# Kernel tuning notes

Hardware: AMD Instinct MI355X
Metric: run time of the kernel (lower is better)

Reference implementation:

```python
import jax, jax.numpy as jnp
import numpy as np

B, S, D = 4, 4096, 2048
K, H = 64, 32
HD = K // H  # 2
LN_EPS = 1e-5


def setup_inputs() -> dict:
    key = jax.random.key(0)
    ks = jax.random.split(key, 8)
    def xavier(k, shape):
        fan_in, fan_out = shape[1], shape[0]
        lim = float(np.sqrt(6.0 / (fan_in + fan_out)))
        return jax.random.uniform(k, shape, jnp.float32, -lim, lim)
    return {
        "x": jax.random.normal(ks[0], (B, S, D), jnp.float32),
        "norm_w": jnp.ones((D,), jnp.float32),
        "norm_b": jnp.zeros((D,), jnp.float32),
        "qkv_w": xavier(ks[1], (3 * K, D)),
        "qkv_b": jnp.zeros((3 * K,), jnp.float32),
        "fm_w": xavier(ks[2], (HD, HD)),
        "fm_b": jnp.zeros((HD,), jnp.float32),
        "out_w": xavier(ks[3], (D, K)),
        "out_b": jnp.zeros((D,), jnp.float32),
    }


def reference(x, norm_w, norm_b, qkv_w, qkv_b, fm_w, fm_b, out_w, out_b):
    # LayerNorm
    mu = jnp.mean(x, axis=-1, keepdims=True)
    var = jnp.var(x, axis=-1, keepdims=True)
    xn = (x - mu) * jax.lax.rsqrt(var + LN_EPS) * norm_w + norm_b
    # QKV projection: [B,S,3K]
    qkv = xn @ qkv_w.T + qkv_b
    q, k, v = jnp.split(qkv, 3, axis=-1)
    # [B,S,K] -> [B,H,S,hd]
    def heads(t):
        return t.reshape(B, S, H, HD).transpose(0, 2, 1, 3)
    q, k, v = heads(q), heads(k), heads(v)
    # feature map: ReLU(Linear)
    q = jax.nn.relu(q @ fm_w.T + fm_b)
    k = jax.nn.relu(k @ fm_w.T + fm_b)
    # linear attention: kv state [B,H,hd,hd]
    kv = jnp.einsum('bhsd,bhse->bhde', k, v)
    attn = jnp.einsum('bhsd,bhde->bhse', q, kv)
    k_sum = jnp.sum(k, axis=2)                      # [B,H,hd]
    q_k_sum = jnp.einsum('bhsd,bhd->bhs', q, k_sum)[..., None]
    attn = attn / (q_k_sum + 1e-8)
    # merge heads -> [B,S,K]
    attn = attn.transpose(0, 2, 1, 3).reshape(B, S, K)
    out = attn @ out_w.T + out_b
    return x + out
```

## Files before the change

### kernel.cpp

```cpp
#include <hip/hip_runtime.h>
#include <hip/hip_bf16.h>
#include <stdint.h>

typedef unsigned short ushort_t;

#define BB 4
#define SS 4096
#define DD 2048
#define KKC 64
#define HH 32
#define NT (BB*SS)
#define NQKV 192
#define QB 64

typedef float f32x4 __attribute__((ext_vector_type(4)));
typedef short s16x8 __attribute__((ext_vector_type(8)));

__device__ __forceinline__ ushort_t f2bf(float f) {
    union { float f; uint32_t u; } c; c.f = f;
    uint32_t u = c.u + 0x7fffu + ((c.u >> 16) & 1u);
    return (ushort_t)(u >> 16);
}
__device__ __forceinline__ float bf2f(ushort_t b) {
    union { uint32_t u; float f; } c; c.u = (uint32_t)b << 16; return c.f;
}

__device__ __forceinline__ uint32_t cvtpk(float lo, float hi) {
    uint32_t r;
    asm("v_cvt_pk_bf16_f32 %0, %1, %2" : "=v"(r) : "v"(lo), "v"(hi));
    return r;
}

__device__ __forceinline__ void mfma16(f32x4& d, s16x8 a, s16x8 b) {
    asm volatile("v_mfma_f32_16x16x32_bf16 %0, %1, %2, %0" : "+v"(d) : "v"(a), "v"(b));
}

__device__ __forceinline__ void gload_lds16(const void* gsrc, void* ldst) {
    __builtin_amdgcn_global_load_lds(
        (const __attribute__((address_space(1))) unsigned int*)gsrc,
        (__attribute__((address_space(3))) unsigned int*)ldst,
        16, 0, 0);
}

__global__ __launch_bounds__(256) void k_pre(
    const float* __restrict__ qkv_w, const float* __restrict__ nw,
    const float* __restrict__ out_w,
    ushort_t* __restrict__ W1, ushort_t* __restrict__ W2) {
    int E = blockIdx.x * 256 + threadIdx.x;
    if (E < 49152) {
        int lane = E & 63; int rest = E >> 6;
        int f = rest % 12, g = rest / 12;
        int col = f * 16 + (lane & 15);
        int k0 = g * 32 + 8 * (lane >> 4);
        const float* src = qkv_w + (size_t)col * DD + k0;
        const float* wp = nw + k0;
        union { ushort_t u[8]; uint4 v; } cv;
        #pragma unroll
        for (int e = 0; e < 8; ++e) cv.u[e] = f2bf(src[e] * wp[e]);
        *(uint4*)(W1 + (size_t)E * 8) = cv.v;
    } else {
        int E2 = E - 49152;
        int lane = E2 & 63; int rest = E2 >> 6;
        int kk = rest & 1, F = rest >> 1;
        int n = F * 16 + (lane & 15);
        int k0 = kk * 32 + 8 * (lane >> 4);
        const float* src = out_w + (size_t)n * KKC + k0;
        union { ushort_t u[8]; uint4 v; } cv;
        #pragma unroll
        for (int e = 0; e < 8; ++e) cv.u[e] = f2bf(src[e]);
        *(uint4*)(W2 + (size_t)E2 * 8) = cv.v;
    }
}

__global__ __launch_bounds__(256) void k_colsum(
    const float* __restrict__ qkv_w, const float* __restrict__ nw,
    const float* __restrict__ nb, const float* __restrict__ qkv_b,
    float* __restrict__ S, float* __restrict__ qb2) {
    int col = blockIdx.x * 4 + (threadIdx.x >> 6);
    int lane = threadIdx.x & 63;
    float s = 0.f, qb = 0.f;
    for (int j = 0; j < 32; ++j) {
        int k = j * 64 + lane;
        float w = qkv_w[(size_t)col * DD + k];
        s += bf2f(f2bf(w * nw[k]));
        qb += nb[k] * w;
    }
    #pragma unroll
    for (int off = 32; off >= 1; off >>= 1) {
        s += __shfl_xor(s, off);
        qb += __shfl_xor(qb, off);
    }
    if (lane == 0) { S[col] = s; qb2[col] = qb + qkv_b[col]; }
}

__global__ __launch_bounds__(512, 2) void k_qkv(
    const float* __restrict__ x, const ushort_t* __restrict__ W1,
    const float* __restrict__ S, const float* __restrict__ qb2,
    const float* __restrict__ fm_w, const float* __restrict__ fm_b,
    float* __restrict__ qfeat,
    float* __restrict__ kvpart)
{
    __shared__ __align__(16) union {
        float xs[2][QB * 16 * 4];
        float cep[QB][NQKV];
    } sm;
    __shared__ float kvred[32][16][6];
    __shared__ float stats2[2][QB][2];
    __shared__ float stats[QB][2];

    const int tid = threadIdx.x;
    const int wave = tid >> 6, lane = tid & 63;
    const int rg = wave & 3, ch = wave >> 2;
    const int m0 = blockIdx.x * QB;

    const int rloc = rg * 16 + (lane & 15);
    const int q4 = lane >> 4;
    const int swz = rloc & 7;

    const int idx0 = wave * 64 + lane;
    const int idx1 = 512 + idx0;
    const int row0 = idx0 >> 4, row1 = idx1 >> 4;
    const size_t xg0 = (size_t)(m0 + row0) * DD + (((idx0 & 15) ^ (row0 & 7)) * 4);
    const size_t xg1 = (size_t)(m0 + row1) * DD + (((idx1 & 15) ^ (row1 & 7)) * 4);
    const int xd0 = (wave * 64) * 16;
    const int xd1 = (512 + wave * 64) * 16;

    const s16x8* __restrict__ Wp = (const s16x8*)W1;
    const int fbase = ch * 6;

    f32x4 acc[6];
    #pragma unroll
    for (int j = 0; j < 6; ++j) acc[j] = (f32x4){0.f, 0.f, 0.f, 0.f};
    float st1 = 0.f, st2 = 0.f;

#define STAGE_X(T, BUF) do { \
        gload_lds16(x + xg0 + (size_t)(T) * 64, (char*)sm.xs[BUF] + xd0); \
        gload_lds16(x + xg1 + (size_t)(T) * 64, (char*)sm.xs[BUF] + xd1); \
    } while (0)

#define LOAD_B(T, DST) do { \
        _Pragma("unroll") \
        for (int kb = 0; kb < 2; ++kb) { \
            _Pragma("unroll") \
            for (int j = 0; j < 6; ++j) \
                DST[kb][j] = Wp[(((size_t)((T) * 2 + kb) * 12) + fbase + j) * 64 + lane]; \
        } \
    } while (0)

#define AFRAG(BUF, DOSTATS) \
        s16x8 afr0, afr1; \
        { \
            const float* base = sm.xs[BUF] + rloc * 64; \
            int sg0 = 2 * q4, sg1 = 8 + 2 * q4; \
            float4 a0 = *(const float4*)(base + ((sg0    ) ^ swz) * 4); \
            float4 a1 = *(const float4*)(base + ((sg0 + 1) ^ swz) * 4); \
            float4 b0 = *(const float4*)(base + ((sg1    ) ^ swz) * 4); \
            float4 b1 = *(const float4*)(base + ((sg1 + 1) ^ swz) * 4); \
            if (DOSTATS) { \
                st1 += a0.x+a0.y+a0.z+a0.w + a1.x+a1.y+a1.z+a1.w \
                     + b0.x+b0.y+b0.z+b0.w + b1.x+b1.y+b1.z+b1.w; \
                st2 += a0.x*a0.x+a0.y*a0.y+a0.z*a0.z+a0.w*a0.w \
                     + a1.x*a1.x+a1.y*a1.y+a1.z*a1.z+a1.w*a1.w \
                     + b0.x*b0.x+b0.y*b0.y+b0.z*b0.z+b0.w*b0.w \
                     + b1.x*b1.x+b1.y*b1.y+b1.z*b1.z+b1.w*b1.w; \
            } \
            union { uint32_t w[4]; s16x8 v; } c0, c1; \
            c0.w[0] = cvtpk(a0.x, a0.y); c0.w[1] = cvtpk(a0.z, a0.w); \
            c0.w[2] = cvtpk(a1.x, a1.y); c0.w[3] = cvtpk(a1.z, a1.w); \
            c1.w[0] = cvtpk(b0.x, b0.y); c1.w[1] = cvtpk(b0.z, b0.w); \
            c1.w[2] = cvtpk(b1.x, b1.y); c1.w[3] = cvtpk(b1.z, b1.w); \
            afr0 = c0.v; afr1 = c1.v; \
        }

    s16x8 bA[2][6], bB[2][6];

    STAGE_X(0, 0);
    LOAD_B(0, bA);

    for (int tp = 0; tp < 16; ++tp) {
        const int t0 = 2 * tp, t1 = 2 * tp + 1;
        __syncthreads();
        STAGE_X(t0 + 1, 1);
        LOAD_B(t0 + 1, bB);
        {
            AFRAG(0, (ch == 0));
            #pragma unroll
            for (int j = 0; j < 6; ++j) {
                mfma16(acc[j], afr0, bA[0][j]);
                mfma16(acc[j], afr1, bA[1][j]);
            }
        }
        __syncthreads();
        if (t1 < 31) {
            STAGE_X(t1 + 1, 0);
            LOAD_B(t1 + 1, bA);
        }
        {
            AFRAG(1, (ch == 1));
            #pragma unroll
            for (int j = 0; j < 6; ++j) {
                mfma16(acc[j], afr0, bB[0][j]);
                mfma16(acc[j], afr1, bB[1][j]);
            }
        }
    }

    st1 += __shfl_xor(st1, 16); st2 += __shfl_xor(st2, 16);
    st1 += __shfl_xor(st1, 32); st2 += __shfl_xor(st2, 32);
    if (lane < 16) { stats2[ch][rloc][0] = st1; stats2[ch][rloc][1] = st2; }
    __syncthreads();

    #pragma unroll
    for (int j = 0; j < 6; ++j) {
        int col = (fbase + j) * 16 + (lane & 15);
        int rbase = rg * 16 + (lane >> 4) * 4;
        #pragma unroll
        for (int r = 0; r < 4; ++r)
            sm.cep[rbase + r][col] = acc[j][r];
    }
    if (tid < QB) {
        float s1 = stats2[0][tid][0] + stats2[1][tid][0];
        float s2 = stats2[0][tid][1] + stats2[1][tid][1];
        float mu = s1 * (1.f / DD);
        float var = s2 * (1.f / DD) - mu * mu;
        stats[tid][0] = mu;
        stats[tid][1] = rsqrtf(var + 1e-5f);
    }
    __syncthreads();

    const int h = tid & 31, gg = tid >> 5;
    const float fm00 = fm_w[0], fm01 = fm_w[1], fm10 = fm_w[2], fm11 = fm_w[3];
    const float fb0 = fm_b[0], fb1 = fm_b[1];
    const float Sq0 = S[2*h],      Sq1 = S[2*h+1],      cq0 = qb2[2*h],      cq1 = qb2[2*h+1];
    const float Sk0 = S[64+2*h],   Sk1 = S[64+2*h+1],   ck0 = qb2[64+2*h],   ck1 = qb2[64+2*h+1];
    const float Sv0 = S[128+2*h],  Sv1 = S[128+2*h+1],  cv0 = qb2[128+2*h],  cv1 = qb2[128+2*h+1];
    float kv00=0, kv01=0, kv10=0, kv11=0, ks0=0, ks1=0;
    #pragma unroll
    for (int i = 0; i < 4; ++i) {
        int tt = gg * 4 + i;
        float mu = stats[tt][0], rs = stats[tt][1];
        float f = mu * rs;
        float q0 = rs * sm.cep[tt][2*h]      - f * Sq0 + cq0;
        float q1 = rs * sm.cep[tt][2*h+1]    - f * Sq1 + cq1;
        float k0 = rs * sm.cep[tt][64+2*h]   - f * Sk0 + ck0;
        float k1 = rs * sm.cep[tt][64+2*h+1] - f * Sk1 + ck1;
        float v0 = rs * sm.cep[tt][128+2*h]  - f * Sv0 + cv0;
        float v1 = rs * sm.cep[tt][128+2*h+1]- f * Sv1 + cv1;
        float qp0 = fmaxf(fm00*q0 + fm01*q1 + fb0, 0.f);
        float qp1 = fmaxf(fm10*q0 + fm11*q1 + fb1, 0.f);
        float kp0 = fmaxf(fm00*k0 + fm01*k1 + fb0, 0.f);
        float kp1 = fmaxf(fm10*k0 + fm11*k1 + fb1, 0.f);
        *(float2*)(qfeat + (size_t)(m0 + tt) * KKC + 2*h) = make_float2(qp0, qp1);
        kv00 += kp0*v0; kv01 += kp0*v1; kv10 += kp1*v0; kv11 += kp1*v1;
        ks0 += kp0; ks1 += kp1;
    }
    kvred[h][gg][0]=kv00; kvred[h][gg][1]=kv01; kvred[h][gg][2]=kv10;
    kvred[h][gg][3]=kv11; kvred[h][gg][4]=ks0;  kvred[h][gg][5]=ks1;
    __syncthreads();
    if (tid < 192) {
        int h2 = tid / 6, j = tid % 6;
        float s = 0.f;
        #pragma unroll
        for (int g2 = 0; g2 < 16; ++g2) s += kvred[h2][g2][j];
        kvpart[(size_t)blockIdx.x * 192 + tid] = s;
    }
#undef STAGE_X
#undef LOAD_B
#undef AFRAG
}

__global__ void k_red(const float* __restrict__ kvpart, float* __restrict__ kvstate) {
    int idx = blockIdx.x * 256 + threadIdx.x;
    if (idx >= BB * HH * 6) return;
    int b = idx / 192, r = idx % 192;
    float s = 0.f;
    for (int blk = 0; blk < 64; ++blk)
        s += kvpart[(size_t)(b * 64 + blk) * 192 + r];
    kvstate[idx] = s;
}

#define CEP_STRIDE 260
__global__ __launch_bounds__(512, 4) void k_out(
    const float* __restrict__ qfeat, const float* __restrict__ kvstate,
    const ushort_t* __restrict__ W2, const float* __restrict__ out_b,
    const float* __restrict__ x, float* __restrict__ out) {
    __shared__ float skv[192];
    __shared__ __align__(16) float cep[32 * CEP_STRIDE];
    const int tid = threadIdx.x, wave = tid >> 6, lane = tid & 63;
    const int rg = wave & 1, cq = wave >> 1;
    const int mb = blockIdx.x >> 1, nb = blockIdx.x & 1;
    const int m0 = mb * 32;
    const int n0 = nb * 1024;
    const int b = m0 >> 12;
    if (tid < 192) skv[tid] = kvstate[b * 192 + tid];

    const int arow = m0 + rg * 16 + (lane & 15);
    const int ksub = 8 * (lane >> 4);
    float4 qa0 = *(const float4*)(qfeat + (size_t)arow * KKC + ksub);
    float4 qa1 = *(const float4*)(qfeat + (size_t)arow * KKC + ksub + 4);
    float4 qb0 = *(const float4*)(qfeat + (size_t)arow * KKC + 32 + ksub);
    float4 qb1 = *(const float4*)(qfeat + (size_t)arow * KKC + 32 + ksub + 4);
    __syncthreads();

    union { ushort_t u[8]; s16x8 v; } ca, cb;
    {
        float qs[8] = {qa0.x,qa0.y,qa0.z,qa0.w,qa1.x,qa1.y,qa1.z,qa1.w};
        float rs[8] = {qb0.x,qb0.y,qb0.z,qb0.w,qb1.x,qb1.y,qb1.z,qb1.w};
        #pragma unroll
        for (int e = 0; e < 8; e += 2) {
            int h = (ksub + e) >> 1;
            const float* kv = skv + h * 6;
            float q0 = qs[e], q1 = qs[e+1];
            float inv = 1.f / (q0 * kv[4] + q1 * kv[5] + 1e-8f);
            ca.u[e]   = f2bf((q0 * kv[0] + q1 * kv[2]) * inv);
            ca.u[e+1] = f2bf((q0 * kv[1] + q1 * kv[3]) * inv);
            const float* kw = skv + (h + 16) * 6;
            float p0 = rs[e], p1 = rs[e+1];
            float iw = 1.f / (p0 * kw[4] + p1 * kw[5] + 1e-8f);
            cb.u[e]   = f2bf((p0 * kw[0] + p1 * kw[2]) * iw);
            cb.u[e+1] = f2bf((p0 * kw[1] + p1 * kw[3]) * iw);
        }
    }

    f32x4 acc[16];
    #pragma unroll
    for (int j = 0; j < 16; ++j) acc[j] = (f32x4){0.f, 0.f, 0.f, 0.f};
    #pragma unroll
    for (int j = 0; j < 16; ++j) {
        int Fg = (n0 >> 4) + cq + 4 * j;
        s16x8 b0 = *(const s16x8*)(W2 + ((size_t)(Fg * 2 + 0) * 64 + lane) * 8);
        s16x8 b1 = *(const s16x8*)(W2 + ((size_t)(Fg * 2 + 1) * 64 + lane) * 8);
        mfma16(acc[j], ca.v, b0);
        mfma16(acc[j], cb.v, b1);
    }

    const int wrow = rg * 16 + 4 * (lane >> 4);
    #pragma unroll
    for (int n = 0; n < 4; ++n) {
        #pragma unroll
        for (int i = 0; i < 4; ++i) {
            int col = cq * 16 + i * 64 + (lane & 15);
            #pragma unroll
            for (int r = 0; r < 4; ++r)
                cep[(wrow + r) * CEP_STRIDE + col] = acc[4 * n + i][r];
        }
        __syncthreads();
        #pragma unroll
        for (int p = 0; p < 4; ++p) {
            int row = p * 8 + (tid >> 6);
            int c4 = tid & 63;
            float4 c = *(const float4*)(cep + row * CEP_STRIDE + c4 * 4);
            int gcol = n0 + n * 256 + c4 * 4;
            size_t off = (size_t)(m0 + row) * DD + gcol;
            float4 xr = *(const float4*)(x + off);
            float4 ob = *(const float4*)(out_b + gcol);
            float4 o;
            o.x = c.x + ob.x + xr.x; o.y = c.y + ob.y + xr.y;
            o.z = c.z + ob.z + xr.z; o.w = c.w + ob.w + xr.w;
            *(float4*)(out + off) = o;
        }
        __syncthreads();
    }
}

extern "C" void kernel_launch(void* const* d_in, const int* in_sizes, int n_in,
                              void* d_out, int out_size, void* d_ws, size_t ws_size,
                              hipStream_t stream) {
    const float* x     = (const float*)d_in[0];
    const float* nw    = (const float*)d_in[1];
    const float* nb    = (const float*)d_in[2];
    const float* qkv_w = (const float*)d_in[3];
    const float* qkv_b = (const float*)d_in[4];
    const float* fm_w  = (const float*)d_in[5];
    const float* fm_b  = (const float*)d_in[6];
    const float* out_w = (const float*)d_in[7];
    const float* out_b = (const float*)d_in[8];
    float* out = (float*)d_out;

    char* ws = (char*)d_ws;
    ushort_t* W1 = (ushort_t*)ws;     ws += (size_t)NQKV * DD * 2;
    ushort_t* W2 = (ushort_t*)ws;     ws += (size_t)DD * KKC * 2;
    float* qfeat = (float*)ws;        ws += (size_t)NT * KKC * 4;
    float* kvpart = (float*)ws;       ws += (size_t)256 * 192 * 4;
    float* kvstate = (float*)ws;      ws += (size_t)BB * HH * 6 * 4;
    float* Svec = (float*)ws;         ws += (size_t)NQKV * 4;
    float* qb2 = (float*)ws;          ws += (size_t)NQKV * 4;

    k_pre<<<256, 256, 0, stream>>>(qkv_w, nw, out_w, W1, W2);
    k_colsum<<<48, 256, 0, stream>>>(qkv_w, nw, nb, qkv_b, Svec, qb2);
    k_qkv<<<NT / QB, 512, 0, stream>>>(x, W1, Svec, qb2, fm_w, fm_b, qfeat, kvpart);
    k_red<<<3, 256, 0, stream>>>(kvpart, kvstate);
    k_out<<<(NT / 32) * 2, 512, 0, stream>>>(qfeat, kvstate, W2, out_b, x, out);
}
```

Measured before the change: 127.8 us.

## Shrink QKV row tile to 16 rows with 4-wave blocks for more parallelism

The fused LayerNorm+QKV kernel now handles 16 rows per block with 256 threads instead of 64 rows with 512 threads. That gives 1024 blocks instead of 256. Each wave now owns 3 of the 12 output column tiles. LayerNorm statistics are split round-robin across the four waves by k-step. The partial kv buffers and the reduction kernel are resized to match. The aim is better spread across CUs and better latency hiding on the x stream, at the cost of each block re-reading the full bf16 QKV weight, which multiplies weight traffic through the cache by four.

```diff
diff --git a/kernel.cpp b/kernel.cpp
--- a/kernel.cpp
+++ b/kernel.cpp
@@ -11,7 +11,7 @@
 #define HH 32
 #define NT (BB*SS)
 #define NQKV 192
-#define QB 64
+#define QB 16
 
 typedef float f32x4 __attribute__((ext_vector_type(4)));
 typedef short s16x8 __attribute__((ext_vector_type(8)));
@@ -93,7 +93,7 @@
     if (lane == 0) { S[col] = s; qb2[col] = qb + qkv_b[col]; }
 }
 
-__global__ __launch_bounds__(512, 2) void k_qkv(
+__global__ __launch_bounds__(256, 4) void k_qkv(
     const float* __restrict__ x, const ushort_t* __restrict__ W1,
     const float* __restrict__ S, const float* __restrict__ qb2,
     const float* __restrict__ fm_w, const float* __restrict__ fm_b,
@@ -101,48 +101,43 @@
     float* __restrict__ kvpart)
 {
     __shared__ __align__(16) union {
-        float xs[2][QB * 16 * 4];
+        float xs[2][QB * 64];
         float cep[QB][NQKV];
     } sm;
-    __shared__ float kvred[32][16][6];
-    __shared__ float stats2[2][QB][2];
+    __shared__ float kvred[32][8][6];
+    __shared__ float stats4[4][QB][2];
     __shared__ float stats[QB][2];
 
     const int tid = threadIdx.x;
     const int wave = tid >> 6, lane = tid & 63;
-    const int rg = wave & 3, ch = wave >> 2;
+    const int ch = wave;
     const int m0 = blockIdx.x * QB;
 
-    const int rloc = rg * 16 + (lane & 15);
+    const int rloc = lane & 15;
     const int q4 = lane >> 4;
     const int swz = rloc & 7;
 
-    const int idx0 = wave * 64 + lane;
-    const int idx1 = 512 + idx0;
-    const int row0 = idx0 >> 4, row1 = idx1 >> 4;
-    const size_t xg0 = (size_t)(m0 + row0) * DD + (((idx0 & 15) ^ (row0 & 7)) * 4);
-    const size_t xg1 = (size_t)(m0 + row1) * DD + (((idx1 & 15) ^ (row1 & 7)) * 4);
+    const int row0 = tid >> 4;
+    const int slot0 = (tid & 15) ^ (row0 & 7);
+    const size_t xg0 = (size_t)(m0 + row0) * DD + slot0 * 4;
     const int xd0 = (wave * 64) * 16;
-    const int xd1 = (512 + wave * 64) * 16;
 
     const s16x8* __restrict__ Wp = (const s16x8*)W1;
-    const int fbase = ch * 6;
-
-    f32x4 acc[6];
-    #pragma unroll
-    for (int j = 0; j < 6; ++j) acc[j] = (f32x4){0.f, 0.f, 0.f, 0.f};
+    const int fbase = ch * 3;
+
+    f32x4 acc[3];
+    #pragma unroll
+    for (int j = 0; j < 3; ++j) acc[j] = (f32x4){0.f, 0.f, 0.f, 0.f};
     float st1 = 0.f, st2 = 0.f;
 
-#define STAGE_X(T, BUF) do { \
-        gload_lds16(x + xg0 + (size_t)(T) * 64, (char*)sm.xs[BUF] + xd0); \
-        gload_lds16(x + xg1 + (size_t)(T) * 64, (char*)sm.xs[BUF] + xd1); \
-    } while (0)
+#define STAGE_X(T, BUF) \
+    gload_lds16(x + xg0 + (size_t)(T) * 64, (char*)sm.xs[BUF] + xd0)
 
 #define LOAD_B(T, DST) do { \
         _Pragma("unroll") \
         for (int kb = 0; kb < 2; ++kb) { \
             _Pragma("unroll") \
-            for (int j = 0; j < 6; ++j) \
+            for (int j = 0; j < 3; ++j) \
                 DST[kb][j] = Wp[(((size_t)((T) * 2 + kb) * 12) + fbase + j) * 64 + lane]; \
         } \
     } while (0)
@@ -172,7 +167,7 @@
             afr0 = c0.v; afr1 = c1.v; \
         }
 
-    s16x8 bA[2][6], bB[2][6];
+    s16x8 bA[2][3], bB[2][3];
 
     STAGE_X(0, 0);
     LOAD_B(0, bA);
@@ -183,9 +178,9 @@
         STAGE_X(t0 + 1, 1);
         LOAD_B(t0 + 1, bB);
         {
-            AFRAG(0, (ch == 0));
+            AFRAG(0, ((t0 & 3) == ch));
             #pragma unroll
-            for (int j = 0; j < 6; ++j) {
+            for (int j = 0; j < 3; ++j) {
                 mfma16(acc[j], afr0, bA[0][j]);
                 mfma16(acc[j], afr1, bA[1][j]);
             }
@@ -196,9 +191,9 @@
             LOAD_B(t1 + 1, bA);
         }
         {
-            AFRAG(1, (ch == 1));
+            AFRAG(1, ((t1 & 3) == ch));
             #pragma unroll
-            for (int j = 0; j < 6; ++j) {
+            for (int j = 0; j < 3; ++j) {
                 mfma16(acc[j], afr0, bB[0][j]);
                 mfma16(acc[j], afr1, bB[1][j]);
             }
@@ -207,20 +202,20 @@
 
     st1 += __shfl_xor(st1, 16); st2 += __shfl_xor(st2, 16);
     st1 += __shfl_xor(st1, 32); st2 += __shfl_xor(st2, 32);
-    if (lane < 16) { stats2[ch][rloc][0] = st1; stats2[ch][rloc][1] = st2; }
+    if (lane < 16) { stats4[ch][lane][0] = st1; stats4[ch][lane][1] = st2; }
     __syncthreads();
 
     #pragma unroll
-    for (int j = 0; j < 6; ++j) {
+    for (int j = 0; j < 3; ++j) {
         int col = (fbase + j) * 16 + (lane & 15);
-        int rbase = rg * 16 + (lane >> 4) * 4;
+        int rbase = (lane >> 4) * 4;
         #pragma unroll
         for (int r = 0; r < 4; ++r)
             sm.cep[rbase + r][col] = acc[j][r];
     }
     if (tid < QB) {
-        float s1 = stats2[0][tid][0] + stats2[1][tid][0];
-        float s2 = stats2[0][tid][1] + stats2[1][tid][1];
+        float s1 = stats4[0][tid][0] + stats4[1][tid][0] + stats4[2][tid][0] + stats4[3][tid][0];
+        float s2 = stats4[0][tid][1] + stats4[1][tid][1] + stats4[2][tid][1] + stats4[3][tid][1];
         float mu = s1 * (1.f / DD);
         float var = s2 * (1.f / DD) - mu * mu;
         stats[tid][0] = mu;
@@ -236,8 +231,8 @@
     const float Sv0 = S[128+2*h],  Sv1 = S[128+2*h+1],  cv0 = qb2[128+2*h],  cv1 = qb2[128+2*h+1];
     float kv00=0, kv01=0, kv10=0, kv11=0, ks0=0, ks1=0;
     #pragma unroll
-    for (int i = 0; i < 4; ++i) {
-        int tt = gg * 4 + i;
+    for (int i = 0; i < 2; ++i) {
+        int tt = gg * 2 + i;
         float mu = stats[tt][0], rs = stats[tt][1];
         float f = mu * rs;
         float q0 = rs * sm.cep[tt][2*h]      - f * Sq0 + cq0;
@@ -261,7 +256,7 @@
         int h2 = tid / 6, j = tid % 6;
         float s = 0.f;
         #pragma unroll
-        for (int g2 = 0; g2 < 16; ++g2) s += kvred[h2][g2][j];
+        for (int g2 = 0; g2 < 8; ++g2) s += kvred[h2][g2][j];
         kvpart[(size_t)blockIdx.x * 192 + tid] = s;
     }
 #undef STAGE_X
@@ -274,8 +269,8 @@
     if (idx >= BB * HH * 6) return;
     int b = idx / 192, r = idx % 192;
     float s = 0.f;
-    for (int blk = 0; blk < 64; ++blk)
-        s += kvpart[(size_t)(b * 64 + blk) * 192 + r];
+    for (int blk = 0; blk < 256; ++blk)
+        s += kvpart[(size_t)(b * 256 + blk) * 192 + r];
     kvstate[idx] = s;
 }
 
@@ -381,14 +376,14 @@
     ushort_t* W1 = (ushort_t*)ws;     ws += (size_t)NQKV * DD * 2;
     ushort_t* W2 = (ushort_t*)ws;     ws += (size_t)DD * KKC * 2;
     float* qfeat = (float*)ws;        ws += (size_t)NT * KKC * 4;
-    float* kvpart = (float*)ws;       ws += (size_t)256 * 192 * 4;
+    float* kvpart = (float*)ws;       ws += (size_t)1024 * 192 * 4;
     float* kvstate = (float*)ws;      ws += (size_t)BB * HH * 6 * 4;
     float* Svec = (float*)ws;         ws += (size_t)NQKV * 4;
     float* qb2 = (float*)ws;          ws += (size_t)NQKV * 4;
 
     k_pre<<<256, 256, 0, stream>>>(qkv_w, nw, out_w, W1, W2);
     k_colsum<<<48, 256, 0, stream>>>(qkv_w, nw, nb, qkv_b, Svec, qb2);
-    k_qkv<<<NT / QB, 512, 0, stream>>>(x, W1, Svec, qb2, fm_w, fm_b, qfeat, kvpart);
+    k_qkv<<<NT / QB, 256, 0, stream>>>(x, W1, Svec, qb2, fm_w, fm_b, qfeat, kvpart);
     k_red<<<3, 256, 0, stream>>>(kvpart, kvstate);
     k_out<<<(NT / 32) * 2, 512, 0, stream>>>(qfeat, kvstate, W2, out_b, x, out);
 }
```

Result: slower. 139.9 us (+9.5%).

## Stage QKV weights through LDS with triple-buffered async pipeline

Applied to the files above, without the earlier changes.

The QKV GEMM kernel now stages both the bf16 weight tile and the x tile into LDS through direct global-to-LDS loads, using three dynamic-shared-memory buffers and a vmcnt-based wait instead of two buffers plus register-held weight fragments. This is meant to keep two tiles in flight ahead of compute and cut VGPR pressure from the prefetched weight registers. In exchange it uses about 120 KB of LDS per block, so only one block fits per CU, and the launch bounds no longer request two blocks per SM. The epilogue reuses the dynamic LDS region for the accumulator scratch.

```diff
diff --git a/kernel.cpp b/kernel.cpp
--- a/kernel.cpp
+++ b/kernel.cpp
@@ -12,6 +12,9 @@
 #define NT (BB*SS)
 #define NQKV 192
 #define QB 64
+
+#define BUFSZ 40960
+#define XOFF  24576
 
 typedef float f32x4 __attribute__((ext_vector_type(4)));
 typedef short s16x8 __attribute__((ext_vector_type(8)));
@@ -93,17 +96,14 @@
     if (lane == 0) { S[col] = s; qb2[col] = qb + qkv_b[col]; }
 }
 
-__global__ __launch_bounds__(512, 2) void k_qkv(
+__global__ __launch_bounds__(512) void k_qkv(
     const float* __restrict__ x, const ushort_t* __restrict__ W1,
     const float* __restrict__ S, const float* __restrict__ qb2,
     const float* __restrict__ fm_w, const float* __restrict__ fm_b,
     float* __restrict__ qfeat,
     float* __restrict__ kvpart)
 {
-    __shared__ __align__(16) union {
-        float xs[2][QB * 16 * 4];
-        float cep[QB][NQKV];
-    } sm;
+    extern __shared__ __align__(16) char dynlds[];
     __shared__ float kvred[32][16][6];
     __shared__ float stats2[2][QB][2];
     __shared__ float stats[QB][2];
@@ -116,107 +116,97 @@
     const int rloc = rg * 16 + (lane & 15);
     const int q4 = lane >> 4;
     const int swz = rloc & 7;
+    const int fbase = ch * 6;
 
     const int idx0 = wave * 64 + lane;
     const int idx1 = 512 + idx0;
     const int row0 = idx0 >> 4, row1 = idx1 >> 4;
     const size_t xg0 = (size_t)(m0 + row0) * DD + (((idx0 & 15) ^ (row0 & 7)) * 4);
     const size_t xg1 = (size_t)(m0 + row1) * DD + (((idx1 & 15) ^ (row1 & 7)) * 4);
-    const int xd0 = (wave * 64) * 16;
-    const int xd1 = (512 + wave * 64) * 16;
-
-    const s16x8* __restrict__ Wp = (const s16x8*)W1;
-    const int fbase = ch * 6;
+    const int xd0 = idx0 * 16 - lane * 16;
+    const int xd1 = idx1 * 16 - lane * 16;
 
     f32x4 acc[6];
     #pragma unroll
     for (int j = 0; j < 6; ++j) acc[j] = (f32x4){0.f, 0.f, 0.f, 0.f};
     float st1 = 0.f, st2 = 0.f;
 
-#define STAGE_X(T, BUF) do { \
-        gload_lds16(x + xg0 + (size_t)(T) * 64, (char*)sm.xs[BUF] + xd0); \
-        gload_lds16(x + xg1 + (size_t)(T) * 64, (char*)sm.xs[BUF] + xd1); \
+#define STAGE(T, OB) do { \
+        char* bB_ = dynlds + (OB); \
+        char* bX_ = dynlds + (OB) + XOFF; \
+        _Pragma("unroll") \
+        for (int i_ = 0; i_ < 3; ++i_) { \
+            int eb_ = i_ * 512 + wave * 64; \
+            gload_lds16((const char*)W1 + ((size_t)(T) * 1536 + eb_ + lane) * 16, \
+                        bB_ + eb_ * 16); \
+        } \
+        gload_lds16(x + xg0 + (size_t)(T) * 64, bX_ + xd0); \
+        gload_lds16(x + xg1 + (size_t)(T) * 64, bX_ + xd1); \
     } while (0)
 
-#define LOAD_B(T, DST) do { \
+#define STEP_BODY(OC, T) do { \
+        const s16x8* bb_ = (const s16x8*)(dynlds + (OC)); \
+        const float* xb_ = (const float*)(dynlds + (OC) + XOFF) + rloc * 64; \
+        const bool doStats_ = (((T) & 1) == ch); \
+        s16x8 afr0_, afr1_; \
+        { \
+            int sg0_ = 2 * q4, sg1_ = 8 + 2 * q4; \
+            float4 a0_ = *(const float4*)(xb_ + ((sg0_    ) ^ swz) * 4); \
+            float4 a1_ = *(const float4*)(xb_ + ((sg0_ + 1) ^ swz) * 4); \
+            float4 b0_ = *(const float4*)(xb_ + ((sg1_    ) ^ swz) * 4); \
+            float4 b1_ = *(const float4*)(xb_ + ((sg1_ + 1) ^ swz) * 4); \
+            if (doStats_) { \
+                st1 += a0_.x+a0_.y+a0_.z+a0_.w + a1_.x+a1_.y+a1_.z+a1_.w \
+                     + b0_.x+b0_.y+b0_.z+b0_.w + b1_.x+b1_.y+b1_.z+b1_.w; \
+                st2 += a0_.x*a0_.x+a0_.y*a0_.y+a0_.z*a0_.z+a0_.w*a0_.w \
+                     + a1_.x*a1_.x+a1_.y*a1_.y+a1_.z*a1_.z+a1_.w*a1_.w \
+                     + b0_.x*b0_.x+b0_.y*b0_.y+b0_.z*b0_.z+b0_.w*b0_.w \
+                     + b1_.x*b1_.x+b1_.y*b1_.y+b1_.z*b1_.z+b1_.w*b1_.w; \
+            } \
+            union { uint32_t w[4]; s16x8 v; } c0_, c1_; \
+            c0_.w[0] = cvtpk(a0_.x, a0_.y); c0_.w[1] = cvtpk(a0_.z, a0_.w); \
+            c0_.w[2] = cvtpk(a1_.x, a1_.y); c0_.w[3] = cvtpk(a1_.z, a1_.w); \
+            c1_.w[0] = cvtpk(b0_.x, b0_.y); c1_.w[1] = cvtpk(b0_.z, b0_.w); \
+            c1_.w[2] = cvtpk(b1_.x, b1_.y); c1_.w[3] = cvtpk(b1_.z, b1_.w); \
+            afr0_ = c0_.v; afr1_ = c1_.v; \
+        } \
         _Pragma("unroll") \
-        for (int kb = 0; kb < 2; ++kb) { \
-            _Pragma("unroll") \
-            for (int j = 0; j < 6; ++j) \
-                DST[kb][j] = Wp[(((size_t)((T) * 2 + kb) * 12) + fbase + j) * 64 + lane]; \
+        for (int j_ = 0; j_ < 6; ++j_) { \
+            s16x8 w0_ = bb_[(fbase + j_) * 64 + lane]; \
+            s16x8 w1_ = bb_[(12 + fbase + j_) * 64 + lane]; \
+            mfma16(acc[j_], afr0_, w0_); \
+            mfma16(acc[j_], afr1_, w1_); \
         } \
     } while (0)
 
-#define AFRAG(BUF, DOSTATS) \
-        s16x8 afr0, afr1; \
-        { \
-            const float* base = sm.xs[BUF] + rloc * 64; \
-            int sg0 = 2 * q4, sg1 = 8 + 2 * q4; \
-            float4 a0 = *(const float4*)(base + ((sg0    ) ^ swz) * 4); \
-            float4 a1 = *(const float4*)(base + ((sg0 + 1) ^ swz) * 4); \
-            float4 b0 = *(const float4*)(base + ((sg1    ) ^ swz) * 4); \
-            float4 b1 = *(const float4*)(base + ((sg1 + 1) ^ swz) * 4); \
-            if (DOSTATS) { \
-                st1 += a0.x+a0.y+a0.z+a0.w + a1.x+a1.y+a1.z+a1.w \
-                     + b0.x+b0.y+b0.z+b0.w + b1.x+b1.y+b1.z+b1.w; \
-                st2 += a0.x*a0.x+a0.y*a0.y+a0.z*a0.z+a0.w*a0.w \
-                     + a1.x*a1.x+a1.y*a1.y+a1.z*a1.z+a1.w*a1.w \
-                     + b0.x*b0.x+b0.y*b0.y+b0.z*b0.z+b0.w*b0.w \
-                     + b1.x*b1.x+b1.y*b1.y+b1.z*b1.z+b1.w*b1.w; \
-            } \
-            union { uint32_t w[4]; s16x8 v; } c0, c1; \
-            c0.w[0] = cvtpk(a0.x, a0.y); c0.w[1] = cvtpk(a0.z, a0.w); \
-            c0.w[2] = cvtpk(a1.x, a1.y); c0.w[3] = cvtpk(a1.z, a1.w); \
-            c1.w[0] = cvtpk(b0.x, b0.y); c1.w[1] = cvtpk(b0.z, b0.w); \
-            c1.w[2] = cvtpk(b1.x, b1.y); c1.w[3] = cvtpk(b1.z, b1.w); \
-            afr0 = c0.v; afr1 = c1.v; \
-        }
-
-    s16x8 bA[2][6], bB[2][6];
-
-    STAGE_X(0, 0);
-    LOAD_B(0, bA);
-
-    for (int tp = 0; tp < 16; ++tp) {
-        const int t0 = 2 * tp, t1 = 2 * tp + 1;
-        __syncthreads();
-        STAGE_X(t0 + 1, 1);
-        LOAD_B(t0 + 1, bB);
-        {
-            AFRAG(0, (ch == 0));
-            #pragma unroll
-            for (int j = 0; j < 6; ++j) {
-                mfma16(acc[j], afr0, bA[0][j]);
-                mfma16(acc[j], afr1, bA[1][j]);
-            }
-        }
-        __syncthreads();
-        if (t1 < 31) {
-            STAGE_X(t1 + 1, 0);
-            LOAD_B(t1 + 1, bA);
-        }
-        {
-            AFRAG(1, (ch == 1));
-            #pragma unroll
-            for (int j = 0; j < 6; ++j) {
-                mfma16(acc[j], afr0, bB[0][j]);
-                mfma16(acc[j], afr1, bB[1][j]);
-            }
-        }
-    }
+    STAGE(0, 0);
+    STAGE(1, BUFSZ);
+
+    unsigned oc = 0, on = BUFSZ, on2 = 2 * BUFSZ;
+    for (int t = 0; t < 31; ++t) {
+        asm volatile("s_waitcnt vmcnt(5)" ::: "memory");
+        __builtin_amdgcn_s_barrier();
+        if (t < 30) STAGE(t + 2, on2);
+        STEP_BODY(oc, t);
+        unsigned tmp = oc; oc = on; on = on2; on2 = tmp;
+    }
+    asm volatile("s_waitcnt vmcnt(0)" ::: "memory");
+    __builtin_amdgcn_s_barrier();
+    STEP_BODY(oc, 31);
 
     st1 += __shfl_xor(st1, 16); st2 += __shfl_xor(st2, 16);
     st1 += __shfl_xor(st1, 32); st2 += __shfl_xor(st2, 32);
     if (lane < 16) { stats2[ch][rloc][0] = st1; stats2[ch][rloc][1] = st2; }
     __syncthreads();
 
+    float (*cep)[NQKV] = (float (*)[NQKV])dynlds;
     #pragma unroll
     for (int j = 0; j < 6; ++j) {
         int col = (fbase + j) * 16 + (lane & 15);
         int rbase = rg * 16 + (lane >> 4) * 4;
         #pragma unroll
         for (int r = 0; r < 4; ++r)
-            sm.cep[rbase + r][col] = acc[j][r];
+            cep[rbase + r][col] = acc[j][r];
     }
     if (tid < QB) {
         float s1 = stats2[0][tid][0] + stats2[1][tid][0];
@@ -240,12 +230,12 @@
         int tt = gg * 4 + i;
         float mu = stats[tt][0], rs = stats[tt][1];
         float f = mu * rs;
-        float q0 = rs * sm.cep[tt][2*h]      - f * Sq0 + cq0;
-        float q1 = rs * sm.cep[tt][2*h+1]    - f * Sq1 + cq1;
-        float k0 = rs * sm.cep[tt][64+2*h]   - f * Sk0 + ck0;
-        float k1 = rs * sm.cep[tt][64+2*h+1] - f * Sk1 + ck1;
-        float v0 = rs * sm.cep[tt][128+2*h]  - f * Sv0 + cv0;
-        float v1 = rs * sm.cep[tt][128+2*h+1]- f * Sv1 + cv1;
+        float q0 = rs * cep[tt][2*h]      - f * Sq0 + cq0;
+        float q1 = rs * cep[tt][2*h+1]    - f * Sq1 + cq1;
+        float k0 = rs * cep[tt][64+2*h]   - f * Sk0 + ck0;
+        float k1 = rs * cep[tt][64+2*h+1] - f * Sk1 + ck1;
+        float v0 = rs * cep[tt][128+2*h]  - f * Sv0 + cv0;
+        float v1 = rs * cep[tt][128+2*h+1]- f * Sv1 + cv1;
         float qp0 = fmaxf(fm00*q0 + fm01*q1 + fb0, 0.f);
         float qp1 = fmaxf(fm10*q0 + fm11*q1 + fb1, 0.f);
         float kp0 = fmaxf(fm00*k0 + fm01*k1 + fb0, 0.f);
@@ -264,9 +254,8 @@
         for (int g2 = 0; g2 < 16; ++g2) s += kvred[h2][g2][j];
         kvpart[(size_t)blockIdx.x * 192 + tid] = s;
     }
-#undef STAGE_X
-#undef LOAD_B
-#undef AFRAG
+#undef STAGE
+#undef STEP_BODY
 }
 
 __global__ void k_red(const float* __restrict__ kvpart, float* __restrict__ kvstate) {
@@ -386,9 +375,12 @@
     float* Svec = (float*)ws;         ws += (size_t)NQKV * 4;
     float* qb2 = (float*)ws;          ws += (size_t)NQKV * 4;
 
+    hipFuncSetAttribute((const void*)k_qkv,
+                        hipFuncAttributeMaxDynamicSharedMemorySize, 3 * BUFSZ);
+
     k_pre<<<256, 256, 0, stream>>>(qkv_w, nw, out_w, W1, W2);
     k_colsum<<<48, 256, 0, stream>>>(qkv_w, nw, nb, qkv_b, Svec, qb2);
-    k_qkv<<<NT / QB, 512, 0, stream>>>(x, W1, Svec, qb2, fm_w, fm_b, qfeat, kvpart);
+    k_qkv<<<NT / QB, 512, 3 * BUFSZ, stream>>>(x, W1, Svec, qb2, fm_w, fm_b, qfeat, kvpart);
     k_red<<<3, 256, 0, stream>>>(kvpart, kvstate);
     k_out<<<(NT / 32) * 2, 512, 0, stream>>>(qfeat, kvstate, W2, out_b, x, out);
 }
```

Result: faster. 124.1 us (-2.9%).

## Replace LDS-staged x loads with per-wave register prefetch and merge small kernels

Applied to the files above, without the earlier changes.

The QKV kernel no longer stages fp32 x through shared memory with async global-to-LDS loads and block-wide barriers. Each wave now loads its own 16 rows into registers, computes the LayerNorm stats there, converts to bf16 and writes a private swizzled double buffer, so the main loop has no __syncthreads. The column-sum kernel is folded into the weight-prep kernel, and the kv reduction kernel is removed: each k_out block sums the 64 partials itself. This cuts two launches and the per-tile barriers, at the cost of more registers and redundant kv reduction work in every k_out block.

```diff
diff --git a/kernel.cpp b/kernel.cpp
--- a/kernel.cpp
+++ b/kernel.cpp
@@ -35,62 +35,55 @@
     asm volatile("v_mfma_f32_16x16x32_bf16 %0, %1, %2, %0" : "+v"(d) : "v"(a), "v"(b));
 }
 
-__device__ __forceinline__ void gload_lds16(const void* gsrc, void* ldst) {
-    __builtin_amdgcn_global_load_lds(
-        (const __attribute__((address_space(1))) unsigned int*)gsrc,
-        (__attribute__((address_space(3))) unsigned int*)ldst,
-        16, 0, 0);
-}
-
 __global__ __launch_bounds__(256) void k_pre(
     const float* __restrict__ qkv_w, const float* __restrict__ nw,
+    const float* __restrict__ nb, const float* __restrict__ qkv_b,
     const float* __restrict__ out_w,
-    ushort_t* __restrict__ W1, ushort_t* __restrict__ W2) {
-    int E = blockIdx.x * 256 + threadIdx.x;
-    if (E < 49152) {
-        int lane = E & 63; int rest = E >> 6;
-        int f = rest % 12, g = rest / 12;
-        int col = f * 16 + (lane & 15);
-        int k0 = g * 32 + 8 * (lane >> 4);
-        const float* src = qkv_w + (size_t)col * DD + k0;
-        const float* wp = nw + k0;
-        union { ushort_t u[8]; uint4 v; } cv;
-        #pragma unroll
-        for (int e = 0; e < 8; ++e) cv.u[e] = f2bf(src[e] * wp[e]);
-        *(uint4*)(W1 + (size_t)E * 8) = cv.v;
+    ushort_t* __restrict__ W1, ushort_t* __restrict__ W2,
+    float* __restrict__ S, float* __restrict__ qb2) {
+    int bid = blockIdx.x;
+    if (bid < 256) {
+        int E = bid * 256 + threadIdx.x;
+        if (E < 49152) {
+            int lane = E & 63; int rest = E >> 6;
+            int f = rest % 12, g = rest / 12;
+            int col = f * 16 + (lane & 15);
+            int k0 = g * 32 + 8 * (lane >> 4);
+            const float* src = qkv_w + (size_t)col * DD + k0;
+            const float* wp = nw + k0;
+            union { ushort_t u[8]; uint4 v; } cv;
+            #pragma unroll
+            for (int e = 0; e < 8; ++e) cv.u[e] = f2bf(src[e] * wp[e]);
+            *(uint4*)(W1 + (size_t)E * 8) = cv.v;
+        } else {
+            int E2 = E - 49152;
+            int lane = E2 & 63; int rest = E2 >> 6;
+            int kk = rest & 1, F = rest >> 1;
+            int n = F * 16 + (lane & 15);
+            int k0 = kk * 32 + 8 * (lane >> 4);
+            const float* src = out_w + (size_t)n * KKC + k0;
+            union { ushort_t u[8]; uint4 v; } cv;
+            #pragma unroll
+            for (int e = 0; e < 8; ++e) cv.u[e] = f2bf(src[e]);
+            *(uint4*)(W2 + (size_t)E2 * 8) = cv.v;
+        }
     } else {
-        int E2 = E - 49152;
-        int lane = E2 & 63; int rest = E2 >> 6;
-        int kk = rest & 1, F = rest >> 1;
-        int n = F * 16 + (lane & 15);
-        int k0 = kk * 32 + 8 * (lane >> 4);
-        const float* src = out_w + (size_t)n * KKC + k0;
-        union { ushort_t u[8]; uint4 v; } cv;
-        #pragma unroll
-        for (int e = 0; e < 8; ++e) cv.u[e] = f2bf(src[e]);
-        *(uint4*)(W2 + (size_t)E2 * 8) = cv.v;
-    }
-}
-
-__global__ __launch_bounds__(256) void k_colsum(
-    const float* __restrict__ qkv_w, const float* __restrict__ nw,
-    const float* __restrict__ nb, const float* __restrict__ qkv_b,
-    float* __restrict__ S, float* __restrict__ qb2) {
-    int col = blockIdx.x * 4 + (threadIdx.x >> 6);
-    int lane = threadIdx.x & 63;
-    float s = 0.f, qb = 0.f;
-    for (int j = 0; j < 32; ++j) {
-        int k = j * 64 + lane;
-        float w = qkv_w[(size_t)col * DD + k];
-        s += bf2f(f2bf(w * nw[k]));
-        qb += nb[k] * w;
-    }
-    #pragma unroll
-    for (int off = 32; off >= 1; off >>= 1) {
-        s += __shfl_xor(s, off);
-        qb += __shfl_xor(qb, off);
-    }
-    if (lane == 0) { S[col] = s; qb2[col] = qb + qkv_b[col]; }
+        int col = (bid - 256) * 4 + (threadIdx.x >> 6);
+        int lane = threadIdx.x & 63;
+        float s = 0.f, qb = 0.f;
+        for (int j = 0; j < 32; ++j) {
+            int k = j * 64 + lane;
+            float w = qkv_w[(size_t)col * DD + k];
+            s += bf2f(f2bf(w * nw[k]));
+            qb += nb[k] * w;
+        }
+        #pragma unroll
+        for (int off = 32; off >= 1; off >>= 1) {
+            s += __shfl_xor(s, off);
+            qb += __shfl_xor(qb, off);
+        }
+        if (lane == 0) { S[col] = s; qb2[col] = qb + qkv_b[col]; }
+    }
 }
 
 __global__ __launch_bounds__(512, 2) void k_qkv(
@@ -101,130 +94,127 @@
     float* __restrict__ kvpart)
 {
     __shared__ __align__(16) union {
-        float xs[2][QB * 16 * 4];
+        ushort_t xb[8][2][16][64];
         float cep[QB][NQKV];
     } sm;
     __shared__ float kvred[32][16][6];
-    __shared__ float stats2[2][QB][2];
     __shared__ float stats[QB][2];
 
     const int tid = threadIdx.x;
     const int wave = tid >> 6, lane = tid & 63;
     const int rg = wave & 3, ch = wave >> 2;
     const int m0 = blockIdx.x * QB;
-
-    const int rloc = rg * 16 + (lane & 15);
-    const int q4 = lane >> 4;
-    const int swz = rloc & 7;
-
-    const int idx0 = wave * 64 + lane;
-    const int idx1 = 512 + idx0;
-    const int row0 = idx0 >> 4, row1 = idx1 >> 4;
-    const size_t xg0 = (size_t)(m0 + row0) * DD + (((idx0 & 15) ^ (row0 & 7)) * 4);
-    const size_t xg1 = (size_t)(m0 + row1) * DD + (((idx1 & 15) ^ (row1 & 7)) * 4);
-    const int xd0 = (wave * 64) * 16;
-    const int xd1 = (512 + wave * 64) * 16;
-
+    const int fbase = ch * 6;
+    const int l15 = lane & 15, q4 = lane >> 4;
+    const bool doStats = (ch == 0);
+
+    const float* xbase = x + (size_t)(m0 + rg * 16 + q4) * DD + l15 * 4;
+    int wb[4];
+    #pragma unroll
+    for (int i = 0; i < 4; ++i) {
+        int r = i * 4 + q4;
+        wb[i] = r * 128 + ((l15 >> 1) ^ (r & 7)) * 16 + (l15 & 1) * 8;
+    }
     const s16x8* __restrict__ Wp = (const s16x8*)W1;
-    const int fbase = ch * 6;
 
     f32x4 acc[6];
     #pragma unroll
     for (int j = 0; j < 6; ++j) acc[j] = (f32x4){0.f, 0.f, 0.f, 0.f};
-    float st1 = 0.f, st2 = 0.f;
-
-#define STAGE_X(T, BUF) do { \
-        gload_lds16(x + xg0 + (size_t)(T) * 64, (char*)sm.xs[BUF] + xd0); \
-        gload_lds16(x + xg1 + (size_t)(T) * 64, (char*)sm.xs[BUF] + xd1); \
-    } while (0)
-
-#define LOAD_B(T, DST) do { \
-        _Pragma("unroll") \
-        for (int kb = 0; kb < 2; ++kb) { \
-            _Pragma("unroll") \
-            for (int j = 0; j < 6; ++j) \
-                DST[kb][j] = Wp[(((size_t)((T) * 2 + kb) * 12) + fbase + j) * 64 + lane]; \
+    float st1[4] = {0.f, 0.f, 0.f, 0.f}, st2[4] = {0.f, 0.f, 0.f, 0.f};
+
+#define LOADX(T, X) do { \
+        _Pragma("unroll") \
+        for (int i_ = 0; i_ < 4; ++i_) \
+            X[i_] = *(const float4*)(xbase + (size_t)(i_ * 4) * DD + (T) * 64); \
+    } while (0)
+
+#define LOADB(T, D) do { \
+        _Pragma("unroll") \
+        for (int kb_ = 0; kb_ < 2; ++kb_) \
+        { _Pragma("unroll") \
+          for (int cf_ = 0; cf_ < 6; ++cf_) \
+            D[kb_][cf_] = Wp[((size_t)(2 * (T) + kb_) * 12 + fbase + cf_) * 64 + lane]; } \
+    } while (0)
+
+#define CVTW(T, X) do { \
+        char* xbw_ = (char*)&sm.xb[wave][(T) & 1][0][0]; \
+        _Pragma("unroll") \
+        for (int i_ = 0; i_ < 4; ++i_) { \
+            if (doStats) { \
+                st1[i_] += X[i_].x + X[i_].y + X[i_].z + X[i_].w; \
+                st2[i_] += X[i_].x*X[i_].x + X[i_].y*X[i_].y \
+                         + X[i_].z*X[i_].z + X[i_].w*X[i_].w; \
+            } \
+            uint2 w_; \
+            w_.x = cvtpk(X[i_].x, X[i_].y); \
+            w_.y = cvtpk(X[i_].z, X[i_].w); \
+            *(uint2*)(xbw_ + wb[i_]) = w_; \
         } \
     } while (0)
 
-#define AFRAG(BUF, DOSTATS) \
-        s16x8 afr0, afr1; \
-        { \
-            const float* base = sm.xs[BUF] + rloc * 64; \
-            int sg0 = 2 * q4, sg1 = 8 + 2 * q4; \
-            float4 a0 = *(const float4*)(base + ((sg0    ) ^ swz) * 4); \
-            float4 a1 = *(const float4*)(base + ((sg0 + 1) ^ swz) * 4); \
-            float4 b0 = *(const float4*)(base + ((sg1    ) ^ swz) * 4); \
-            float4 b1 = *(const float4*)(base + ((sg1 + 1) ^ swz) * 4); \
-            if (DOSTATS) { \
-                st1 += a0.x+a0.y+a0.z+a0.w + a1.x+a1.y+a1.z+a1.w \
-                     + b0.x+b0.y+b0.z+b0.w + b1.x+b1.y+b1.z+b1.w; \
-                st2 += a0.x*a0.x+a0.y*a0.y+a0.z*a0.z+a0.w*a0.w \
-                     + a1.x*a1.x+a1.y*a1.y+a1.z*a1.z+a1.w*a1.w \
-                     + b0.x*b0.x+b0.y*b0.y+b0.z*b0.z+b0.w*b0.w \
-                     + b1.x*b1.x+b1.y*b1.y+b1.z*b1.z+b1.w*b1.w; \
-            } \
-            union { uint32_t w[4]; s16x8 v; } c0, c1; \
-            c0.w[0] = cvtpk(a0.x, a0.y); c0.w[1] = cvtpk(a0.z, a0.w); \
-            c0.w[2] = cvtpk(a1.x, a1.y); c0.w[3] = cvtpk(a1.z, a1.w); \
-            c1.w[0] = cvtpk(b0.x, b0.y); c1.w[1] = cvtpk(b0.z, b0.w); \
-            c1.w[2] = cvtpk(b1.x, b1.y); c1.w[3] = cvtpk(b1.z, b1.w); \
-            afr0 = c0.v; afr1 = c1.v; \
-        }
-
-    s16x8 bA[2][6], bB[2][6];
-
-    STAGE_X(0, 0);
-    LOAD_B(0, bA);
+#define AREAD(T, AF) do { \
+        const char* xbr_ = (const char*)&sm.xb[wave][(T) & 1][0][0]; \
+        _Pragma("unroll") \
+        for (int kb_ = 0; kb_ < 2; ++kb_) \
+            AF[kb_] = *(const s16x8*)(xbr_ + l15 * 128 + (((kb_ * 4 + q4) ^ (l15 & 7)) << 4)); \
+    } while (0)
+
+#define MM(AF, D) do { \
+        _Pragma("unroll") \
+        for (int kb_ = 0; kb_ < 2; ++kb_) \
+        { _Pragma("unroll") \
+          for (int cf_ = 0; cf_ < 6; ++cf_) \
+            mfma16(acc[cf_], AF[kb_], D[kb_][cf_]); } \
+    } while (0)
+
+    float4 xA[4], xB[4];
+    s16x8 Ba[2][6], Bb[2][6], af[2];
+
+    LOADX(0, xA);
+    LOADB(0, Ba);
+    CVTW(0, xA);
 
     for (int tp = 0; tp < 16; ++tp) {
-        const int t0 = 2 * tp, t1 = 2 * tp + 1;
-        __syncthreads();
-        STAGE_X(t0 + 1, 1);
-        LOAD_B(t0 + 1, bB);
-        {
-            AFRAG(0, (ch == 0));
-            #pragma unroll
-            for (int j = 0; j < 6; ++j) {
-                mfma16(acc[j], afr0, bA[0][j]);
-                mfma16(acc[j], afr1, bA[1][j]);
+        const int t0 = 2 * tp, t1 = t0 + 1;
+        LOADX(t1, xB); LOADB(t1, Bb);
+        AREAD(t0, af); MM(af, Ba);
+        CVTW(t1, xB);
+        if (t1 < 31) { LOADX(t1 + 1, xA); LOADB(t1 + 1, Ba); }
+        AREAD(t1, af); MM(af, Bb);
+        if (t1 < 31) CVTW(t1 + 1, xA);
+    }
+#undef LOADX
+#undef LOADB
+#undef CVTW
+#undef AREAD
+#undef MM
+
+    if (doStats) {
+        #pragma unroll
+        for (int i = 0; i < 4; ++i) {
+            float s1 = st1[i], s2 = st2[i];
+            s1 += __shfl_xor(s1, 1); s2 += __shfl_xor(s2, 1);
+            s1 += __shfl_xor(s1, 2); s2 += __shfl_xor(s2, 2);
+            s1 += __shfl_xor(s1, 4); s2 += __shfl_xor(s2, 4);
+            s1 += __shfl_xor(s1, 8); s2 += __shfl_xor(s2, 8);
+            if (l15 == 0) {
+                int row = rg * 16 + i * 4 + q4;
+                float mu = s1 * (1.f / DD);
+                float var = s2 * (1.f / DD) - mu * mu;
+                stats[row][0] = mu;
+                stats[row][1] = rsqrtf(var + 1e-5f);
             }
         }
-        __syncthreads();
-        if (t1 < 31) {
-            STAGE_X(t1 + 1, 0);
-            LOAD_B(t1 + 1, bA);
-        }
-        {
-            AFRAG(1, (ch == 1));
-            #pragma unroll
-            for (int j = 0; j < 6; ++j) {
-                mfma16(acc[j], afr0, bB[0][j]);
-                mfma16(acc[j], afr1, bB[1][j]);
-            }
-        }
-    }
-
-    st1 += __shfl_xor(st1, 16); st2 += __shfl_xor(st2, 16);
-    st1 += __shfl_xor(st1, 32); st2 += __shfl_xor(st2, 32);
-    if (lane < 16) { stats2[ch][rloc][0] = st1; stats2[ch][rloc][1] = st2; }
+    }
     __syncthreads();
 
     #pragma unroll
     for (int j = 0; j < 6; ++j) {
-        int col = (fbase + j) * 16 + (lane & 15);
-        int rbase = rg * 16 + (lane >> 4) * 4;
+        int col = (fbase + j) * 16 + l15;
+        int rbase = rg * 16 + q4 * 4;
         #pragma unroll
         for (int r = 0; r < 4; ++r)
             sm.cep[rbase + r][col] = acc[j][r];
-    }
-    if (tid < QB) {
-        float s1 = stats2[0][tid][0] + stats2[1][tid][0];
-        float s2 = stats2[0][tid][1] + stats2[1][tid][1];
-        float mu = s1 * (1.f / DD);
-        float var = s2 * (1.f / DD) - mu * mu;
-        stats[tid][0] = mu;
-        stats[tid][1] = rsqrtf(var + 1e-5f);
     }
     __syncthreads();
 
@@ -264,24 +254,11 @@
         for (int g2 = 0; g2 < 16; ++g2) s += kvred[h2][g2][j];
         kvpart[(size_t)blockIdx.x * 192 + tid] = s;
     }
-#undef STAGE_X
-#undef LOAD_B
-#undef AFRAG
-}
-
-__global__ void k_red(const float* __restrict__ kvpart, float* __restrict__ kvstate) {
-    int idx = blockIdx.x * 256 + threadIdx.x;
-    if (idx >= BB * HH * 6) return;
-    int b = idx / 192, r = idx % 192;
-    float s = 0.f;
-    for (int blk = 0; blk < 64; ++blk)
-        s += kvpart[(size_t)(b * 64 + blk) * 192 + r];
-    kvstate[idx] = s;
 }
 
 #define CEP_STRIDE 260
 __global__ __launch_bounds__(512, 4) void k_out(
-    const float* __restrict__ qfeat, const float* __restrict__ kvstate,
+    const float* __restrict__ qfeat, const float* __restrict__ kvpart,
     const ushort_t* __restrict__ W2, const float* __restrict__ out_b,
     const float* __restrict__ x, float* __restrict__ out) {
     __shared__ float skv[192];
@@ -292,7 +269,14 @@
     const int m0 = mb * 32;
     const int n0 = nb * 1024;
     const int b = m0 >> 12;
-    if (tid < 192) skv[tid] = kvstate[b * 192 + tid];
+
+    if (tid < 192) {
+        float s = 0.f;
+        #pragma unroll 8
+        for (int j = 0; j < 64; ++j)
+            s += kvpart[(size_t)(b * 64 + j) * 192 + tid];
+        skv[tid] = s;
+    }
 
     const int arow = m0 + rg * 16 + (lane & 15);
     const int ksub = 8 * (lane >> 4);
@@ -382,13 +366,10 @@
     ushort_t* W2 = (ushort_t*)ws;     ws += (size_t)DD * KKC * 2;
     float* qfeat = (float*)ws;        ws += (size_t)NT * KKC * 4;
     float* kvpart = (float*)ws;       ws += (size_t)256 * 192 * 4;
-    float* kvstate = (float*)ws;      ws += (size_t)BB * HH * 6 * 4;
     float* Svec = (float*)ws;         ws += (size_t)NQKV * 4;
     float* qb2 = (float*)ws;          ws += (size_t)NQKV * 4;
 
-    k_pre<<<256, 256, 0, stream>>>(qkv_w, nw, out_w, W1, W2);
-    k_colsum<<<48, 256, 0, stream>>>(qkv_w, nw, nb, qkv_b, Svec, qb2);
+    k_pre<<<304, 256, 0, stream>>>(qkv_w, nw, nb, qkv_b, out_w, W1, W2, Svec, qb2);
     k_qkv<<<NT / QB, 512, 0, stream>>>(x, W1, Svec, qb2, fm_w, fm_b, qfeat, kvpart);
-    k_red<<<3, 256, 0, stream>>>(kvpart, kvstate);
-    k_out<<<(NT / 32) * 2, 512, 0, stream>>>(qfeat, kvstate, W2, out_b, x, out);
-}
+    k_out<<<(NT / 32) * 2, 512, 0, stream>>>(qfeat, kvpart, W2, out_b, x, out);
+}
```

Result: faster. 121.2 us (-5.1%).
